# Kernel optimization log

Measured on AMD Instinct MI355X. Metric: run time of the kernel, lower is better.

## Reference

```python
import jax, jax.numpy as jnp
import numpy as np

MIN_EXPERTS = 1
MAX_EXPERTS = 8
TEMPERATURE = 1.0


def setup_inputs() -> dict:
    key = jax.random.key(0)
    ks = jax.random.split(key, 7)
    B, S, H, E = 8, 4096, 1024, 64
    Hh = H // 2
    return {
        "hidden_states": jax.random.normal(ks[0], (B, S, H), dtype=jnp.float32),
        "W_router": jax.random.normal(ks[1], (E, H), dtype=jnp.float32) * 0.02,
        "b_router": jax.random.normal(ks[2], (E,), dtype=jnp.float32) * 0.02,
        "W1": jax.random.normal(ks[3], (Hh, H), dtype=jnp.float32) * 0.02,
        "b1": jax.random.normal(ks[4], (Hh,), dtype=jnp.float32) * 0.02,
        "W2": jax.random.normal(ks[5], (1, Hh), dtype=jnp.float32) * 0.02,
        "b2": jax.random.normal(ks[6], (1,), dtype=jnp.float32) * 0.02,
    }


def reference(hidden_states, W_router, b_router, W1, b1, W2, b2):
    B, S, H = hidden_states.shape
    flat = hidden_states.reshape(-1, H)                     # [N, H]

    # router logits
    router_logits = (flat @ W_router.T + b_router) / TEMPERATURE  # [N, E]

    # confidence net: Linear -> ReLU -> Linear -> Sigmoid
    h = jax.nn.relu(flat @ W1.T + b1)                       # [N, H/2]
    confidence = jax.nn.sigmoid(h @ W2.T + b2).squeeze(-1)  # [N]

    # dynamic k per token (torch.round = half-to-even, same as jnp.round)
    dk = MIN_EXPERTS + (MAX_EXPERTS - MIN_EXPERTS) * (1.0 - confidence)
    dk = jnp.clip(jnp.round(dk), MIN_EXPERTS, MAX_EXPERTS).astype(jnp.int32)  # [N]

    routing_probs = jax.nn.softmax(router_logits, axis=-1)  # [N, E]

    # single top-k pass replaces per-iteration sort; mask slots >= dynamic_k
    top_vals, top_idx = jax.lax.top_k(routing_probs, MAX_EXPERTS)  # [N, max_k]
    slot = jnp.arange(MAX_EXPERTS, dtype=jnp.int32)[None, :]       # [1, max_k]
    active = slot < dk[:, None]                                    # [N, max_k]
    sel_w = jnp.where(active, top_vals, 0.0)
    sel_i = jnp.where(active, top_idx, 0).astype(jnp.int64)

    sel_w = sel_w.reshape(B, S, MAX_EXPERTS)
    sel_i = sel_i.reshape(B, S, MAX_EXPERTS)
    return sel_w, sel_i, confidence, router_logits
```

## Files before the change

### kernel.cpp

```cpp
#include <hip/hip_runtime.h>
#include <hip/hip_bf16.h>
#include <math.h>

#define N_TOK 32768
#define HDIM 1024
#define HH 512
#define NOUT 576
#define BM 128
#define BN 64
#define BK 32
#define THREADS 256
#define KC 384

#define OFF_SELW 0
#define OFF_SELI 262144
#define OFF_CONF 524288
#define OFF_LOG  557056

__device__ float  g_Bmat[HDIM * NOUT];
__device__ double g_partial[N_TOK * 8];

__global__ __launch_bounds__(256) void k_build(const float* __restrict__ W1,
                                               const float* __restrict__ Wr) {
  int idx = blockIdx.x * 256 + threadIdx.x;
  int k = idx / NOUT;
  int j = idx - k * NOUT;
  float v = (j < HH) ? W1[(size_t)j * HDIM + k] : Wr[(size_t)(j - HH) * HDIM + k];
  g_Bmat[idx] = v;
}

__global__ __launch_bounds__(THREADS) void k_gemm(const float* __restrict__ A,
                                                  const float* __restrict__ b1,
                                                  const float* __restrict__ W2,
                                                  const float* __restrict__ b_router,
                                                  float* __restrict__ out_logits) {
  __shared__ float As[BK][BM];
  __shared__ float Bs[BK][BN];

  int bid = blockIdx.x;
  int xcd = bid & 7;
  int s   = bid >> 3;
  int j   = s % 9;
  int t   = xcd + 8 * (s / 9);

  const int tid = threadIdx.x;
  const int tx  = tid & 15;
  const int ty  = tid >> 4;
  const int m0  = t * BM;
  const int n0  = j * BN;

  float acc[8][4];
  float carry[8][4];
  #pragma unroll
  for (int i = 0; i < 8; ++i)
    #pragma unroll
    for (int c = 0; c < 4; ++c) { acc[i][c] = 0.f; carry[i][c] = 0.f; }

  const int arow = tid >> 1;
  const int akc  = tid & 1;
  const float* Ag = A + (size_t)(m0 + arow) * HDIM + akc * 16;

  for (int k0 = 0; k0 < HDIM; k0 += BK) {
    if (k0 == KC || k0 == 2 * KC) {
      #pragma unroll
      for (int i = 0; i < 8; ++i)
        #pragma unroll
        for (int c = 0; c < 4; ++c) {
          carry[i][c] = carry[i][c] + acc[i][c];
          acc[i][c] = 0.f;
        }
    }

    float4 av[4];
    #pragma unroll
    for (int c = 0; c < 4; ++c)
      av[c] = *(const float4*)(Ag + k0 + c * 4);
    float4 bv[2];
    #pragma unroll
    for (int c = 0; c < 2; ++c) {
      int idx = tid + c * 256;
      int kr  = idx >> 4;
      int ch  = idx & 15;
      bv[c] = *(const float4*)&g_Bmat[(size_t)(k0 + kr) * NOUT + n0 + ch * 4];
    }
    __syncthreads();
    #pragma unroll
    for (int c = 0; c < 4; ++c) {
      int kb = akc * 16 + c * 4;
      As[kb + 0][arow] = av[c].x;
      As[kb + 1][arow] = av[c].y;
      As[kb + 2][arow] = av[c].z;
      As[kb + 3][arow] = av[c].w;
    }
    #pragma unroll
    for (int c = 0; c < 2; ++c) {
      int idx = tid + c * 256;
      int kr  = idx >> 4;
      int ch  = idx & 15;
      *(float4*)&Bs[kr][ch * 4] = bv[c];
    }
    __syncthreads();

    #pragma unroll 4
    for (int kk = 0; kk < BK; ++kk) {
      float4 a03 = *(const float4*)&As[kk][ty * 8 + 0];
      float4 a47 = *(const float4*)&As[kk][ty * 8 + 4];
      float a[8] = {a03.x, a03.y, a03.z, a03.w, a47.x, a47.y, a47.z, a47.w};
      float b[4];
      b[0] = Bs[kk][tx * 4 + 0];
      b[1] = Bs[kk][tx * 4 + 1];
      b[2] = Bs[kk][tx * 4 + 2];
      b[3] = Bs[kk][tx * 4 + 3];
      #pragma unroll
      for (int i = 0; i < 8; ++i)
        #pragma unroll
        for (int c = 0; c < 4; ++c)
          acc[i][c] = fmaf(a[i], b[c], acc[i][c]);
    }
  }

  float res[8][4];
  #pragma unroll
  for (int i = 0; i < 8; ++i)
    #pragma unroll
    for (int c = 0; c < 4; ++c) res[i][c] = carry[i][c] + acc[i][c];

  if (j < 8) {
    double w2v[4];
    float  b1v[4];
    #pragma unroll
    for (int c = 0; c < 4; ++c) {
      w2v[c] = (double)W2[n0 + tx * 4 + c];
      b1v[c] = b1[n0 + tx * 4 + c];
    }
    #pragma unroll
    for (int i = 0; i < 8; ++i) {
      double sacc = 0.0;
      #pragma unroll
      for (int c = 0; c < 4; ++c) {
        float h = fmaxf(res[i][c] + b1v[c], 0.f);
        sacc = fma((double)h, w2v[c], sacc);
      }
      sacc += __shfl_xor(sacc, 1, 64);
      sacc += __shfl_xor(sacc, 2, 64);
      sacc += __shfl_xor(sacc, 4, 64);
      sacc += __shfl_xor(sacc, 8, 64);
      if (tx == 0) g_partial[(size_t)(m0 + ty * 8 + i) * 8 + j] = sacc;
    }
  } else {
    float brv[4];
    #pragma unroll
    for (int c = 0; c < 4; ++c) brv[c] = b_router[tx * 4 + c];
    #pragma unroll
    for (int i = 0; i < 8; ++i) {
      int row = m0 + ty * 8 + i;
      float o[4];
      #pragma unroll
      for (int c = 0; c < 4; ++c) o[c] = res[i][c] + brv[c];
      *(float4*)&out_logits[(size_t)row * 64 + tx * 4] =
          make_float4(o[0], o[1], o[2], o[3]);
    }
  }
}

__global__ __launch_bounds__(256) void k_post(const float* __restrict__ b2,
                                              float* __restrict__ d_out) {
  int tk = blockIdx.x * 256 + threadIdx.x;

  double ca = (double)b2[0];
  #pragma unroll
  for (int jj = 0; jj < 8; ++jj) ca += g_partial[(size_t)tk * 8 + jj];
  double conf = 1.0 / (1.0 + exp(-ca));
  double dkf  = 1.0 + 7.0 * (1.0 - conf);
  double dkr  = rint(dkf);
  int dk = (int)fmin(fmax(dkr, 1.0), 8.0);

  const float* logits = d_out + OFF_LOG + (size_t)tk * 64;
  float l[64];
  #pragma unroll
  for (int e4 = 0; e4 < 16; ++e4)
    *(float4*)&l[e4 * 4] = *(const float4*)&logits[e4 * 4];

  float mx = l[0];
  #pragma unroll
  for (int e = 1; e < 64; ++e) mx = fmaxf(mx, l[e]);

  float ex[64];
  #pragma unroll
  for (int e = 0; e < 64; ++e) ex[e] = expf(l[e] - mx);

  float r[8];
  #pragma unroll
  for (int q = 0; q < 8; ++q) r[q] = ex[q];
  #pragma unroll
  for (int b = 1; b < 8; ++b)
    #pragma unroll
    for (int q = 0; q < 8; ++q) r[q] += ex[b * 8 + q];
  float ssum = ((r[0] + r[1]) + (r[2] + r[3])) + ((r[4] + r[5]) + (r[6] + r[7]));

  float v[64];
  #pragma unroll
  for (int e = 0; e < 64; ++e) v[e] = ex[e] / ssum;

  float* sel_w = d_out + OFF_SELW + (size_t)tk * 8;
  float* sel_i = d_out + OFF_SELI + (size_t)tk * 8;
  unsigned long long used = 0ull;
  #pragma unroll
  for (int slot = 0; slot < 8; ++slot) {
    float best = -1.f;
    int   bi   = 0;
    #pragma unroll
    for (int e = 0; e < 64; ++e) {
      bool ok = (((used >> e) & 1ull) == 0ull) && (v[e] > best);
      best = ok ? v[e] : best;
      bi   = ok ? e    : bi;
    }
    used |= (1ull << bi);
    bool active = slot < dk;
    sel_w[slot] = active ? best : 0.f;
    sel_i[slot] = active ? (float)bi : 0.f;
  }
  d_out[OFF_CONF + tk] = (float)conf;
}

extern "C" void kernel_launch(void* const* d_in, const int* in_sizes, int n_in,
                              void* d_out, int out_size, void* d_ws, size_t ws_size,
                              hipStream_t stream) {
  const float* hidden   = (const float*)d_in[0];
  const float* W_router = (const float*)d_in[1];
  const float* b_router = (const float*)d_in[2];
  const float* W1       = (const float*)d_in[3];
  const float* b1       = (const float*)d_in[4];
  const float* W2       = (const float*)d_in[5];
  const float* b2       = (const float*)d_in[6];
  float* out = (float*)d_out;

  k_build<<<(HDIM * NOUT) / 256, 256, 0, stream>>>(W1, W_router);
  k_gemm<<<(N_TOK / BM) * 9, THREADS, 0, stream>>>(hidden, b1, W2, b_router,
                                                   out + OFF_LOG);
  k_post<<<N_TOK / 256, 256, 0, stream>>>(b2, out);
}
```

Baseline: 687.2 us.

## Enlarge GEMM tile to 256x64 with 8x8 per-thread microtiles

```diff
diff --git a/kernel.cpp b/kernel.cpp
--- a/kernel.cpp
+++ b/kernel.cpp
@@ -6,7 +6,7 @@
 #define HDIM 1024
 #define HH 512
 #define NOUT 576
-#define BM 128
+#define BM 256
 #define BN 64
 #define BK 32
 #define THREADS 256
@@ -29,11 +29,11 @@
   g_Bmat[idx] = v;
 }
 
-__global__ __launch_bounds__(THREADS) void k_gemm(const float* __restrict__ A,
-                                                  const float* __restrict__ b1,
-                                                  const float* __restrict__ W2,
-                                                  const float* __restrict__ b_router,
-                                                  float* __restrict__ out_logits) {
+__global__ __launch_bounds__(THREADS, 2) void k_gemm(const float* __restrict__ A,
+                                                     const float* __restrict__ b1,
+                                                     const float* __restrict__ W2,
+                                                     const float* __restrict__ b_router,
+                                                     float* __restrict__ out_logits) {
   __shared__ float As[BK][BM];
   __shared__ float Bs[BK][BN];
 
@@ -44,36 +44,34 @@
   int t   = xcd + 8 * (s / 9);
 
   const int tid = threadIdx.x;
-  const int tx  = tid & 15;
-  const int ty  = tid >> 4;
+  const int tx  = tid & 7;
+  const int ty  = tid >> 3;
   const int m0  = t * BM;
   const int n0  = j * BN;
 
-  float acc[8][4];
-  float carry[8][4];
+  float acc[8][8];
+  float carry[8][8];
   #pragma unroll
   for (int i = 0; i < 8; ++i)
     #pragma unroll
-    for (int c = 0; c < 4; ++c) { acc[i][c] = 0.f; carry[i][c] = 0.f; }
-
-  const int arow = tid >> 1;
-  const int akc  = tid & 1;
-  const float* Ag = A + (size_t)(m0 + arow) * HDIM + akc * 16;
+    for (int c = 0; c < 8; ++c) { acc[i][c] = 0.f; carry[i][c] = 0.f; }
+
+  const float* Ag = A + (size_t)(m0 + tid) * HDIM;
 
   for (int k0 = 0; k0 < HDIM; k0 += BK) {
     if (k0 == KC || k0 == 2 * KC) {
       #pragma unroll
       for (int i = 0; i < 8; ++i)
         #pragma unroll
-        for (int c = 0; c < 4; ++c) {
+        for (int c = 0; c < 8; ++c) {
           carry[i][c] = carry[i][c] + acc[i][c];
           acc[i][c] = 0.f;
         }
     }
 
-    float4 av[4];
-    #pragma unroll
-    for (int c = 0; c < 4; ++c)
+    float4 av[8];
+    #pragma unroll
+    for (int c = 0; c < 8; ++c)
       av[c] = *(const float4*)(Ag + k0 + c * 4);
     float4 bv[2];
     #pragma unroll
@@ -85,12 +83,12 @@
     }
     __syncthreads();
     #pragma unroll
-    for (int c = 0; c < 4; ++c) {
-      int kb = akc * 16 + c * 4;
-      As[kb + 0][arow] = av[c].x;
-      As[kb + 1][arow] = av[c].y;
-      As[kb + 2][arow] = av[c].z;
-      As[kb + 3][arow] = av[c].w;
+    for (int c = 0; c < 8; ++c) {
+      int kb = c * 4;
+      As[kb + 0][tid] = av[c].x;
+      As[kb + 1][tid] = av[c].y;
+      As[kb + 2][tid] = av[c].z;
+      As[kb + 3][tid] = av[c].w;
     }
     #pragma unroll
     for (int c = 0; c < 2; ++c) {
@@ -105,66 +103,63 @@
     for (int kk = 0; kk < BK; ++kk) {
       float4 a03 = *(const float4*)&As[kk][ty * 8 + 0];
       float4 a47 = *(const float4*)&As[kk][ty * 8 + 4];
+      float4 b03 = *(const float4*)&Bs[kk][tx * 8 + 0];
+      float4 b47 = *(const float4*)&Bs[kk][tx * 8 + 4];
       float a[8] = {a03.x, a03.y, a03.z, a03.w, a47.x, a47.y, a47.z, a47.w};
-      float b[4];
-      b[0] = Bs[kk][tx * 4 + 0];
-      b[1] = Bs[kk][tx * 4 + 1];
-      b[2] = Bs[kk][tx * 4 + 2];
-      b[3] = Bs[kk][tx * 4 + 3];
+      float b[8] = {b03.x, b03.y, b03.z, b03.w, b47.x, b47.y, b47.z, b47.w};
       #pragma unroll
       for (int i = 0; i < 8; ++i)
         #pragma unroll
-        for (int c = 0; c < 4; ++c)
+        for (int c = 0; c < 8; ++c)
           acc[i][c] = fmaf(a[i], b[c], acc[i][c]);
     }
   }
 
-  float res[8][4];
   #pragma unroll
   for (int i = 0; i < 8; ++i)
     #pragma unroll
-    for (int c = 0; c < 4; ++c) res[i][c] = carry[i][c] + acc[i][c];
+    for (int c = 0; c < 8; ++c) carry[i][c] = carry[i][c] + acc[i][c];
 
   if (j < 8) {
-    double w2v[4];
-    float  b1v[4];
-    #pragma unroll
-    for (int c = 0; c < 4; ++c) {
-      w2v[c] = (double)W2[n0 + tx * 4 + c];
-      b1v[c] = b1[n0 + tx * 4 + c];
+    double w2v[8];
+    float  b1v[8];
+    #pragma unroll
+    for (int c = 0; c < 8; ++c) {
+      w2v[c] = (double)W2[n0 + tx * 8 + c];
+      b1v[c] = b1[n0 + tx * 8 + c];
     }
     #pragma unroll
     for (int i = 0; i < 8; ++i) {
       double sacc = 0.0;
       #pragma unroll
-      for (int c = 0; c < 4; ++c) {
-        float h = fmaxf(res[i][c] + b1v[c], 0.f);
+      for (int c = 0; c < 8; ++c) {
+        float h = fmaxf(carry[i][c] + b1v[c], 0.f);
         sacc = fma((double)h, w2v[c], sacc);
       }
       sacc += __shfl_xor(sacc, 1, 64);
       sacc += __shfl_xor(sacc, 2, 64);
       sacc += __shfl_xor(sacc, 4, 64);
-      sacc += __shfl_xor(sacc, 8, 64);
       if (tx == 0) g_partial[(size_t)(m0 + ty * 8 + i) * 8 + j] = sacc;
     }
   } else {
-    float brv[4];
-    #pragma unroll
-    for (int c = 0; c < 4; ++c) brv[c] = b_router[tx * 4 + c];
+    float brv[8];
+    #pragma unroll
+    for (int c = 0; c < 8; ++c) brv[c] = b_router[tx * 8 + c];
     #pragma unroll
     for (int i = 0; i < 8; ++i) {
       int row = m0 + ty * 8 + i;
-      float o[4];
-      #pragma unroll
-      for (int c = 0; c < 4; ++c) o[c] = res[i][c] + brv[c];
-      *(float4*)&out_logits[(size_t)row * 64 + tx * 4] =
-          make_float4(o[0], o[1], o[2], o[3]);
+      float o[8];
+      #pragma unroll
+      for (int c = 0; c < 8; ++c) o[c] = carry[i][c] + brv[c];
+      float* dst = out_logits + (size_t)row * 64 + tx * 8;
+      *(float4*)dst       = make_float4(o[0], o[1], o[2], o[3]);
+      *(float4*)(dst + 4) = make_float4(o[4], o[5], o[6], o[7]);
     }
   }
 }
 
-__global__ __launch_bounds__(256) void k_post(const float* __restrict__ b2,
-                                              float* __restrict__ d_out) {
+__global__ __launch_bounds__(256, 2) void k_post(const float* __restrict__ b2,
+                                                 float* __restrict__ d_out) {
   int tk = blockIdx.x * 256 + threadIdx.x;
 
   double ca = (double)b2[0];
@@ -176,31 +171,29 @@
   int dk = (int)fmin(fmax(dkr, 1.0), 8.0);
 
   const float* logits = d_out + OFF_LOG + (size_t)tk * 64;
-  float l[64];
+  float x[64];
   #pragma unroll
   for (int e4 = 0; e4 < 16; ++e4)
-    *(float4*)&l[e4 * 4] = *(const float4*)&logits[e4 * 4];
-
-  float mx = l[0];
-  #pragma unroll
-  for (int e = 1; e < 64; ++e) mx = fmaxf(mx, l[e]);
-
-  float ex[64];
-  #pragma unroll
-  for (int e = 0; e < 64; ++e) ex[e] = expf(l[e] - mx);
+    *(float4*)&x[e4 * 4] = *(const float4*)&logits[e4 * 4];
+
+  float mx = x[0];
+  #pragma unroll
+  for (int e = 1; e < 64; ++e) mx = fmaxf(mx, x[e]);
+
+  #pragma unroll
+  for (int e = 0; e < 64; ++e) x[e] = expf(x[e] - mx);
 
   float r[8];
   #pragma unroll
-  for (int q = 0; q < 8; ++q) r[q] = ex[q];
+  for (int q = 0; q < 8; ++q) r[q] = x[q];
   #pragma unroll
   for (int b = 1; b < 8; ++b)
     #pragma unroll
-    for (int q = 0; q < 8; ++q) r[q] += ex[b * 8 + q];
+    for (int q = 0; q < 8; ++q) r[q] += x[b * 8 + q];
   float ssum = ((r[0] + r[1]) + (r[2] + r[3])) + ((r[4] + r[5]) + (r[6] + r[7]));
 
-  float v[64];
-  #pragma unroll
-  for (int e = 0; e < 64; ++e) v[e] = ex[e] / ssum;
+  #pragma unroll
+  for (int e = 0; e < 64; ++e) x[e] = x[e] / ssum;
 
   float* sel_w = d_out + OFF_SELW + (size_t)tk * 8;
   float* sel_i = d_out + OFF_SELI + (size_t)tk * 8;
@@ -211,8 +204,8 @@
     int   bi   = 0;
     #pragma unroll
     for (int e = 0; e < 64; ++e) {
-      bool ok = (((used >> e) & 1ull) == 0ull) && (v[e] > best);
-      best = ok ? v[e] : best;
+      bool ok = (((used >> e) & 1ull) == 0ull) && (x[e] > best);
+      best = ok ? x[e] : best;
       bi   = ok ? e    : bi;
     }
     used |= (1ull << bi);
```

Result: no change. 699.0 us (+1.7%).
